# Performance work log

Measured on AMD Instinct MI355X. Metric: run time of the kernel, lower is better.

The kernel has to match this reference:

```python
import jax, jax.numpy as jnp
import numpy as np

N_NODES = 20000
N_EDGES = 320000
N_GRAPHS = 256
D = 256
L = 4
EPS = 1e-5


def setup_inputs() -> dict:
    key = jax.random.key(0)
    ks = jax.random.split(key, 20)
    x = jax.random.normal(ks[0], (N_NODES, D), dtype=jnp.float32)
    edge_index = jax.random.randint(ks[1], (2, N_EDGES), 0, N_NODES, dtype=jnp.int64)
    batch = jnp.sort(jax.random.randint(ks[2], (N_NODES,), 0, N_GRAPHS, dtype=jnp.int64))
    s = 1.0 / np.sqrt(D)
    Wl = jax.random.uniform(ks[3], (L, D, D), jnp.float32, -s, s)
    bl = jax.random.uniform(ks[4], (L, D), jnp.float32, -s, s)
    Wr = jax.random.uniform(ks[5], (L, D, D), jnp.float32, -s, s)
    gamma = jnp.ones((L, D), jnp.float32)
    beta = jnp.zeros((L, D), jnp.float32)
    fc1_w = jax.random.uniform(ks[6], (D, 128), jnp.float32, -s, s)
    fc1_b = jax.random.uniform(ks[7], (128,), jnp.float32, -s, s)
    s2 = 1.0 / np.sqrt(128)
    fc2_w = jax.random.uniform(ks[8], (128, 64), jnp.float32, -s2, s2)
    fc2_b = jax.random.uniform(ks[9], (64,), jnp.float32, -s2, s2)
    s3 = 1.0 / np.sqrt(64)
    fc3_w = jax.random.uniform(ks[10], (64, 10), jnp.float32, -s3, s3)
    fc3_b = jax.random.uniform(ks[11], (10,), jnp.float32, -s3, s3)
    return dict(x=x, edge_index=edge_index, batch=batch, Wl=Wl, bl=bl, Wr=Wr,
                gamma=gamma, beta=beta, fc1_w=fc1_w, fc1_b=fc1_b,
                fc2_w=fc2_w, fc2_b=fc2_b, fc3_w=fc3_w, fc3_b=fc3_b)


def reference(x, edge_index, batch, Wl, bl, Wr, gamma, beta,
              fc1_w, fc1_b, fc2_w, fc2_b, fc3_w, fc3_b):
    src, dst = edge_index[0], edge_index[1]
    # in-degree for mean aggregation (zero-degree nodes -> 0 aggregate)
    deg = jax.ops.segment_sum(jnp.ones((src.shape[0],), x.dtype), dst, num_segments=N_NODES)
    inv_deg = jnp.where(deg > 0, 1.0 / jnp.maximum(deg, 1.0), 0.0)[:, None]
    for i in range(L):
        # SAGEConv: mean-aggregate neighbors, then lin_l(agg) + lin_r(x)
        agg = jax.ops.segment_sum(x[src], dst, num_segments=N_NODES) * inv_deg
        h = agg @ Wl[i] + bl[i] + x @ Wr[i]
        # BatchNorm (training mode: biased batch statistics over nodes)
        mu = jnp.mean(h, axis=0)
        var = jnp.mean(jnp.square(h - mu), axis=0)
        h = (h - mu) * jax.lax.rsqrt(var + EPS) * gamma[i] + beta[i]
        x = jax.nn.relu(h)
    # global_mean_pool over graphs
    cnt = jax.ops.segment_sum(jnp.ones((N_NODES,), x.dtype), batch, num_segments=N_GRAPHS)
    g = jax.ops.segment_sum(x, batch, num_segments=N_GRAPHS) / jnp.maximum(cnt, 1.0)[:, None]
    # MLP classifier: 256 -> 128 -> 64 -> 10
    g = jax.nn.relu(g @ fc1_w + fc1_b)
    g = jax.nn.relu(g @ fc2_w + fc2_b)
    return g @ fc3_w + fc3_b
```

## Files before the change

kernel.cpp:

```cpp
#include <hip/hip_runtime.h>
#include <hip/hip_bf16.h>

#define NN 20000
#define NE 320000
#define NG 256
#define DD 256
#define NL 4
#define NBX2 157
#define NBKT 79

typedef __attribute__((ext_vector_type(8))) short short8;
typedef __attribute__((ext_vector_type(4))) float float4_t;

__device__ __forceinline__ int ld_idx(const int* __restrict__ p, int i, int f64) {
    return f64 ? p[2 * i] : p[i];
}

__device__ __forceinline__ float bf2f(ushort u) {
    return __uint_as_float(((unsigned)u) << 16);
}

__device__ __forceinline__ ushort f2bf(float f) {
    __hip_bfloat16 b = __float2bfloat16(f);
    return *(ushort*)&b;
}


__global__ void k_init(const int* __restrict__ ei, const int* __restrict__ batch,
                       const ushort* __restrict__ x, int* __restrict__ flags,
                       int* __restrict__ deg) {
    int gid = blockIdx.x * 256 + threadIdx.x;
    for (int i = gid; i < NN; i += gridDim.x * 256) deg[i] = 0;
    if (blockIdx.x == 0) {
        __shared__ int cnt0, cnt1, weird;
        int t = threadIdx.x;
        if (t == 0) { cnt0 = 0; cnt1 = 0; weird = 0; }
        __syncthreads();
        for (int tt = t; tt < 512; tt += 256) {
            if (ei[2 * tt + 1] != 0) atomicAdd(&cnt0, 1);
            int i = tt * 9;
            if (batch[2 * i + 1] != 0) atomicAdd(&cnt1, 1);
#pragma unroll
            for (int j = 0; j < 16; j++) {
                ushort v = x[tt * 16 + j];
                if (((v >> 7) & 0xFF) >= 0xC0) atomicAdd(&weird, 1);
            }
        }
        __syncthreads();
        if (t == 0) {
            flags[0] = (cnt0 == 0) ? 1 : 0;
            flags[1] = (cnt1 == 0) ? 1 : 0;
            flags[2] = (weird == 0) ? 1 : 0;
        }
    }
}


#define POFF_BL   0
#define POFF_GA   1024
#define POFF_BE   2048
#define POFF_F1W  3072
#define POFF_F1B  35840
#define POFF_F2W  35968
#define POFF_F2B  44160
#define POFF_F3W  44224
#define POFF_F3B  44864
#define PTOT      44874

#define NB_CVT8   2500
#define NB_FRAG   128
#define NB_CVTP   176
#define NB_DEG    1250
#define NB_GST    79
#define B_FRAG    (NB_CVT8)
#define B_CVTP    (B_FRAG + NB_FRAG)
#define B_DEG     (B_CVTP + NB_CVTP)
#define B_GST     (B_DEG + NB_DEG)
#define NB_PREP   (B_GST + NB_GST)


__global__ __launch_bounds__(256) void k_prep(
    const void* __restrict__ x_in, const void* __restrict__ WL,
    const void* __restrict__ WR, const int* __restrict__ ei,
    const int* __restrict__ batch,
    const void* s0, const void* s1, const void* s2, const void* s3,
    const void* s4, const void* s5, const void* s6, const void* s7, const void* s8,
    ushort* __restrict__ xcan, ushort* __restrict__ wtL, ushort* __restrict__ wtR,
    ushort* __restrict__ pcan, int* __restrict__ deg, int* __restrict__ gstart,
    const int* __restrict__ fl) {
    int blk = blockIdx.x;
    int t = threadIdx.x;
    if (blk < B_FRAG) {
        int i = blk * 256 + t;
        if (fl[2]) {
            *(int4*)(xcan + (size_t)i * 8) = ((const int4*)x_in)[i];
        } else {
            const float* f = (const float*)x_in + (size_t)i * 8;
            ushort ov[8];
#pragma unroll
            for (int d = 0; d < 8; d++) ov[d] = f2bf(f[d]);
            *(int4*)(xcan + (size_t)i * 8) = *(int4*)ov;
        }
    } else if (blk < B_CVTP) {
        __shared__ ushort T[64][65];
        int bid = blk - B_FRAG;
        int lm = bid >> 4;
        int tile = bid & 15;
        int tk = (tile >> 2) * 64, tn = (tile & 3) * 64;
        const void* W = (lm >= 4) ? WR : WL;
        ushort* Wt = (lm >= 4) ? wtR : wtL;
        size_t base = (size_t)(lm & 3) << 16;
        int f32 = !fl[2];
#pragma unroll
        for (int i = 0; i < 16; i++) {
            int flat = t + i * 256;
            int r = flat >> 6, c = flat & 63;
            size_t src = base + (size_t)(tk + r) * 256 + tn + c;
            ushort v = f32 ? f2bf(((const float*)W)[src]) : ((const ushort*)W)[src];
            T[c][r] = v;
        }
        __syncthreads();
#pragma unroll
        for (int i = 0; i < 2; i++) {
            int slot = t + i * 256;
            int f = slot >> 6;
            int lane = slot & 63;
            int ln = (f >> 1) * 16 + (lane & 15);
            int lk = (f & 1) * 32 + ((lane >> 4) << 3);
            int gfblk = ((tn + ln) >> 4) * 8 + ((tk + lk) >> 5);
            ushort tmp[8];
#pragma unroll
            for (int j = 0; j < 8; j++) tmp[j] = T[ln][lk + j];
            *(int4*)(Wt + base + (size_t)gfblk * 512 + lane * 8) = *(int4*)tmp;
        }
    } else if (blk < B_DEG) {
        int i = (blk - B_CVTP) * 256 + t;
        if (i >= PTOT) return;
        const int offs[10] = {POFF_BL, POFF_GA, POFF_BE, POFF_F1W, POFF_F1B,
                              POFF_F2W, POFF_F2B, POFF_F3W, POFF_F3B, PTOT};
        const void* srcs[9] = {s0, s1, s2, s3, s4, s5, s6, s7, s8};
        int seg = 0;
#pragma unroll
        for (int k = 1; k < 9; k++) if (i >= offs[k]) seg = k;
        int local = i - offs[seg];
        if (fl[2]) pcan[i] = ((const ushort*)srcs[seg])[local];
        else       pcan[i] = f2bf(((const float*)srcs[seg])[local]);
    } else if (blk < B_GST) {
        int e = (blk - B_DEG) * 256 + t;
        if (e < NE) {
            int src = ld_idx(ei, e, fl[0]);
            int dst = ld_idx(ei, NE + e, fl[0]);
            if ((unsigned)dst < NN && (unsigned)src < NN) atomicAdd(&deg[dst], 1);
        }
    } else {
        int i = (blk - B_GST) * 256 + t;
        if (i >= NN) return;
        int b = ld_idx(batch, i, fl[1]);
        int bp = (i == 0) ? -1 : ld_idx(batch, i - 1, fl[1]);
        for (int g = bp + 1; g <= b; g++)
            if ((unsigned)g <= NG) gstart[g] = i;
        if (i == NN - 1)
            for (int g = b + 1; g <= NG; g++) gstart[g] = NN;
    }
}


__global__ __launch_bounds__(256) void k_scanA(const int* __restrict__ deg,
                                               int* __restrict__ bsum) {
    __shared__ int red[256];
    int t = threadIdx.x;
    int node = blockIdx.x * 256 + t;
    red[t] = (node < NN) ? deg[node] : 0;
    __syncthreads();
    for (int off = 128; off; off >>= 1) {
        if (t < off) red[t] += red[t + off];
        __syncthreads();
    }
    if (t == 0) bsum[blockIdx.x] = red[0];
}

__global__ __launch_bounds__(256) void k_scanC(
    const int* __restrict__ deg, const int* __restrict__ bsum,
    int* __restrict__ rowst, int* __restrict__ cursor, float* __restrict__ invdeg) {
    __shared__ int bpart[128];
    __shared__ int part[256];
    int b = blockIdx.x, t = threadIdx.x;
    if (t < 128) {
        int s = (t < NBKT) ? bsum[t] : 0;
        bpart[t] = s;
    }
    __syncthreads();
    for (int off = 1; off < 128; off <<= 1) {
        int v = 0;
        if (t < 128 && t >= off) v = bpart[t - off];
        __syncthreads();
        if (t < 128) bpart[t] += v;
        __syncthreads();
    }
    int bpref = (b == 0) ? 0 : bpart[b - 1];
    if (b == 0 && t == 0) rowst[NN] = bpart[NBKT - 1];
    int node = b * 256 + t;
    int d = (node < NN) ? deg[node] : 0;
    part[t] = d;
    __syncthreads();
    for (int off = 1; off < 256; off <<= 1) {
        int v = (t >= off) ? part[t - off] : 0;
        __syncthreads();
        part[t] += v;
        __syncthreads();
    }
    if (node < NN) {
        int o = bpref + part[t] - d;
        rowst[node] = o;
        cursor[node] = o;
        invdeg[node] = d > 0 ? 1.0f / (float)d : 0.0f;
    }
}

__global__ void k_fill(const int* __restrict__ ei, int* __restrict__ cursor,
                       int* __restrict__ csr, const int* __restrict__ fl) {
    int e = blockIdx.x * 256 + threadIdx.x;
    if (e < NE) {
        int src = ld_idx(ei, e, fl[0]);
        int dst = ld_idx(ei, NE + e, fl[0]);
        if ((unsigned)dst < NN && (unsigned)src < NN) {
            int p = atomicAdd(&cursor[dst], 1);
            if ((unsigned)p < NE) csr[p] = src;
        }
    }
}


template <int BNF>
__global__ __launch_bounds__(256) void k_agg4(
    const ushort* __restrict__ X, const int* __restrict__ rs,
    const int* __restrict__ csr, const float* __restrict__ invdeg,
    const float* __restrict__ bnsc, const float* __restrict__ bnsh,
    ushort* __restrict__ AGG) {
    int node = blockIdx.x * 4 + (threadIdx.x >> 6);
    if (node >= NN) return;
    int h = (threadIdx.x >> 5) & 1;
    int j = threadIdx.x & 31;
    float sc[8], sh[8];
    if (BNF) {
        float4 a0 = *(const float4*)(bnsc + j * 8);
        float4 a1 = *(const float4*)(bnsc + j * 8 + 4);
        float4 b0 = *(const float4*)(bnsh + j * 8);
        float4 b1 = *(const float4*)(bnsh + j * 8 + 4);
        sc[0] = a0.x; sc[1] = a0.y; sc[2] = a0.z; sc[3] = a0.w;
        sc[4] = a1.x; sc[5] = a1.y; sc[6] = a1.z; sc[7] = a1.w;
        sh[0] = b0.x; sh[1] = b0.y; sh[2] = b0.z; sh[3] = b0.w;
        sh[4] = b1.x; sh[5] = b1.y; sh[6] = b1.z; sh[7] = b1.w;
    }
    int e0 = rs[node], e1 = rs[node + 1];
    float acc[8] = {};
    int e = e0 + h;
    for (; e + 14 < e1; e += 16) {
        int4 v[8];
#pragma unroll
        for (int r = 0; r < 8; r++) {
            int s = csr[e + 2 * r];
            v[r] = *(const int4*)(X + (size_t)s * DD + j * 8);
        }
#pragma unroll
        for (int r = 0; r < 8; r++) {
            const ushort* u = (const ushort*)&v[r];
#pragma unroll
            for (int d = 0; d < 8; d++) {
                float x = bf2f(u[d]);
                if (BNF) x = fmaxf(x * sc[d] + sh[d], 0.0f);
                acc[d] += x;
            }
        }
    }
    for (; e + 2 < e1; e += 4) {
        int sA = csr[e], sB = csr[e + 2];
        int4 vA = *(const int4*)(X + (size_t)sA * DD + j * 8);
        int4 vB = *(const int4*)(X + (size_t)sB * DD + j * 8);
        const ushort* uA = (const ushort*)&vA;
        const ushort* uB = (const ushort*)&vB;
#pragma unroll
        for (int d = 0; d < 8; d++) {
            float xA = bf2f(uA[d]), xB = bf2f(uB[d]);
            if (BNF) {
                xA = fmaxf(xA * sc[d] + sh[d], 0.0f);
                xB = fmaxf(xB * sc[d] + sh[d], 0.0f);
            }
            acc[d] += xA + xB;
        }
    }
    for (; e < e1; e += 2) {
        int s = csr[e];
        int4 v = *(const int4*)(X + (size_t)s * DD + j * 8);
        const ushort* u = (const ushort*)&v;
#pragma unroll
        for (int d = 0; d < 8; d++) {
            float x = bf2f(u[d]);
            if (BNF) x = fmaxf(x * sc[d] + sh[d], 0.0f);
            acc[d] += x;
        }
    }
#pragma unroll
    for (int d = 0; d < 8; d++)
        acc[d] += __shfl_down(acc[d], 32);
    if (h == 0) {
        float inv = invdeg[node];
        ushort ov[8];
#pragma unroll
        for (int d = 0; d < 8; d++) ov[d] = f2bf(acc[d] * inv);
        *(int4*)(AGG + (size_t)node * DD + j * 8) = *(int4*)ov;
    }
}


template <int BNF>
__global__ __launch_bounds__(256) void k_gemm5(
    const ushort* __restrict__ A1, const ushort* __restrict__ A2,
    const ushort* __restrict__ WtF1, const ushort* __restrict__ WtF2,
    const ushort* __restrict__ bias,
    const float* __restrict__ bnsc, const float* __restrict__ bnsh,
    ushort* __restrict__ H, float* __restrict__ psum, float* __restrict__ psq) {
    __shared__ ushort Als[128][40];
    __shared__ float colsum[128];
    __shared__ float colsq[128];
    const int m0 = blockIdx.x * 128;
    const int n0 = blockIdx.y * 128;
    const int tid = threadIdx.x;
    const int w = tid >> 6, l = tid & 63, lr = l & 15, q = l >> 4;
    const int wm = (w >> 1) * 64, wn = (w & 1) * 64;
    float4_t acc[4][4] = {};

    const int srow = tid >> 1;
    const int sce = (tid & 1) * 16;
    const int nb8 = ((n0 + wn) >> 4) * 8;

    for (int mat = 0; mat < 2; ++mat) {
        const ushort* A = mat ? A2 : A1;
        const ushort* Wf = mat ? WtF2 : WtF1;
        for (int k0 = 0; k0 < 256; k0 += 32) {
            int ar = m0 + srow; if (ar >= NN) ar = NN - 1;
            int4 av0 = *(const int4*)(A + (size_t)ar * DD + k0 + sce);
            int4 av1 = *(const int4*)(A + (size_t)ar * DD + k0 + sce + 8);
            if (BNF && mat == 1) {
                float scv[16], shv[16];
#pragma unroll
                for (int g = 0; g < 4; g++) {
                    float4 s4 = *(const float4*)(bnsc + k0 + sce + g * 4);
                    float4 h4 = *(const float4*)(bnsh + k0 + sce + g * 4);
                    scv[g*4] = s4.x; scv[g*4+1] = s4.y; scv[g*4+2] = s4.z; scv[g*4+3] = s4.w;
                    shv[g*4] = h4.x; shv[g*4+1] = h4.y; shv[g*4+2] = h4.z; shv[g*4+3] = h4.w;
                }
                ushort* u0 = (ushort*)&av0;
                ushort* u1 = (ushort*)&av1;
#pragma unroll
                for (int d = 0; d < 8; d++) {
                    u0[d] = f2bf(fmaxf(bf2f(u0[d]) * scv[d] + shv[d], 0.0f));
                    u1[d] = f2bf(fmaxf(bf2f(u1[d]) * scv[8 + d] + shv[8 + d], 0.0f));
                }
            }
            *(int4*)&Als[srow][sce] = av0;
            *(int4*)&Als[srow][sce + 8] = av1;
            const ushort* bbase = Wf + (((size_t)(nb8 + (k0 >> 5))) << 9) + l * 8;
            short8 bf[4];
#pragma unroll
            for (int in = 0; in < 4; in++)
                bf[in] = *(const short8*)(bbase + in * 4096);
            __syncthreads();
            short8 af[4];
#pragma unroll
            for (int im = 0; im < 4; im++)
                af[im] = *(const short8*)&Als[wm + im * 16 + lr][q * 8];
#pragma unroll
            for (int im = 0; im < 4; im++)
#pragma unroll
                for (int in = 0; in < 4; in++)
                    acc[im][in] = __builtin_amdgcn_mfma_f32_16x16x32_bf16(
                        af[im], bf[in], acc[im][in], 0, 0, 0);
            __syncthreads();
        }
    }
    if (tid < 128) { colsum[tid] = 0.0f; colsq[tid] = 0.0f; }
    __syncthreads();

    int mbase = m0 + wm + q * 4;
#pragma unroll
    for (int in = 0; in < 4; in++) {
        int n = n0 + wn + in * 16 + lr;
        float b = bf2f(bias[n]);
        float s = 0.0f, s2 = 0.0f;
#pragma unroll
        for (int im = 0; im < 4; im++) {
#pragma unroll
            for (int i = 0; i < 4; i++) {
                int m = mbase + im * 16 + i;
                if (m < NN) {
                    float hv = acc[im][in][i] + b;
                    ushort hb = f2bf(hv);
                    H[(size_t)m * DD + n] = hb;
                    float hq = bf2f(hb);
                    s += hq;
                    s2 += hq * hq;
                }
            }
        }
        s += __shfl_xor(s, 16);  s += __shfl_xor(s, 32);
        s2 += __shfl_xor(s2, 16); s2 += __shfl_xor(s2, 32);
        if (q == 0) {
            atomicAdd(&colsum[wn + in * 16 + lr], s);
            atomicAdd(&colsq[wn + in * 16 + lr], s2);
        }
    }
    __syncthreads();
    if (tid < 128) {
        psum[(size_t)blockIdx.x * DD + n0 + tid] = colsum[tid];
        psq[(size_t)blockIdx.x * DD + n0 + tid] = colsq[tid];
    }
}


__global__ __launch_bounds__(64) void k_bnfinal3(
    const float* __restrict__ psum, const float* __restrict__ psq,
    const ushort* __restrict__ gamma, const ushort* __restrict__ beta,
    float* __restrict__ scale, float* __restrict__ shift) {
    int c = blockIdx.x;
    int t = threadIdx.x;
    float s = 0.0f, s2 = 0.0f;
    for (int b = t; b < NBX2; b += 64) {
        s += psum[(size_t)b * DD + c];
        s2 += psq[(size_t)b * DD + c];
    }
#pragma unroll
    for (int o = 32; o; o >>= 1) {
        s += __shfl_down(s, o);
        s2 += __shfl_down(s2, o);
    }
    if (t == 0) {
        float mu = s * (1.0f / NN);
        float var = s2 * (1.0f / NN) - mu * mu;
        if (var < 0.0f) var = 0.0f;
        float rstd = rsqrtf(var + 1e-5f);
        float g = bf2f(gamma[c]);
        float b2 = bf2f(beta[c]);
        scale[c] = g * rstd;
        shift[c] = b2 - mu * g * rstd;
    }
}


__global__ __launch_bounds__(256) void k_head(
    const ushort* __restrict__ Hb, const float* __restrict__ scale,
    const float* __restrict__ shift, const int* __restrict__ gstart,
    const ushort* __restrict__ fc1w, const ushort* __restrict__ fc1b,
    const ushort* __restrict__ fc2w, const ushort* __restrict__ fc2b,
    const ushort* __restrict__ fc3w, const ushort* __restrict__ fc3b,
    void* __restrict__ out, const int* __restrict__ fl) {
    __shared__ float g[256];
    __shared__ float h1[128];
    __shared__ float h2[64];
    int gid = blockIdx.x;
    int t = threadIdx.x;
    int s0 = gstart[gid], e = gstart[gid + 1];
    float sc = scale[t], sh = shift[t];
    float acc = 0.0f;
    for (int i = s0; i < e; i++)
        acc += fmaxf(bf2f(Hb[(size_t)i * DD + t]) * sc + sh, 0.0f);
    g[t] = acc / fmaxf((float)(e - s0), 1.0f);
    __syncthreads();
    if (t < 128) {
        float a = bf2f(fc1b[t]);
        for (int k = 0; k < 256; k++)
            a += g[k] * bf2f(fc1w[k * 128 + t]);
        h1[t] = fmaxf(a, 0.0f);
    }
    __syncthreads();
    if (t < 64) {
        float a2 = bf2f(fc2b[t]);
        for (int k = 0; k < 128; k++)
            a2 += h1[k] * bf2f(fc2w[k * 64 + t]);
        h2[t] = fmaxf(a2, 0.0f);
    }
    __syncthreads();
    if (t < 10) {
        float a3 = bf2f(fc3b[t]);
        for (int k = 0; k < 64; k++)
            a3 += h2[k] * bf2f(fc3w[k * 10 + t]);
        if (fl[2]) ((__hip_bfloat16*)out)[gid * 10 + t] = __float2bfloat16(a3);
        else       ((float*)out)[gid * 10 + t] = a3;
    }
}


static inline char* bump(char*& p, size_t n) {
    char* r = p;
    p += (n + 255) & ~(size_t)255;
    return r;
}

extern "C" void kernel_launch(void* const* d_in, const int* in_sizes, int n_in,
                              void* d_out, int out_size, void* d_ws, size_t ws_size,
                              hipStream_t stream) {
    const void* x_in  = d_in[0];
    const int*  ei    = (const int*)d_in[1];
    const int*  batch = (const int*)d_in[2];
    const void* Wl    = d_in[3];
    const void* bl    = d_in[4];
    const void* Wr    = d_in[5];
    const void* gamma = d_in[6];
    const void* beta  = d_in[7];

    char* p = (char*)d_ws;
    int*    flags    = (int*)bump(p, 256);
    ushort* wtL      = (ushort*)bump(p, (size_t)NL * 65536 * 2);
    ushort* wtR      = (ushort*)bump(p, (size_t)NL * 65536 * 2);
    ushort* xcan     = (ushort*)bump(p, (size_t)NN * DD * 2);
    ushort* pcan     = (ushort*)bump(p, (size_t)PTOT * 2);
    int*    deg      = (int*)bump(p, NN * 4);
    int*    bsum     = (int*)bump(p, NBKT * 4);
    int*    rowst    = (int*)bump(p, (NN + 1) * 4);
    int*    cursor   = (int*)bump(p, NN * 4);
    float*  invdeg   = (float*)bump(p, NN * 4);
    int*    csr      = (int*)bump(p, NE * 4);
    int*    gstart   = (int*)bump(p, (NG + 1) * 4);
    ushort* agg      = (ushort*)bump(p, (size_t)NN * DD * 2);
    ushort* hb0      = (ushort*)bump(p, (size_t)NN * DD * 2);
    ushort* hb1      = (ushort*)bump(p, (size_t)NN * DD * 2);
    float*  psum     = (float*)bump(p, (size_t)NBX2 * DD * 4);
    float*  psq      = (float*)bump(p, (size_t)NBX2 * DD * 4);
    float*  scale    = (float*)bump(p, DD * 4);
    float*  shift    = (float*)bump(p, DD * 4);

    if ((size_t)(p - (char*)d_ws) > ws_size) return;

    ushort* blc = pcan + POFF_BL;
    ushort* gac = pcan + POFF_GA;
    ushort* bec = pcan + POFF_BE;
    ushort* f1w = pcan + POFF_F1W;
    ushort* f1b = pcan + POFF_F1B;
    ushort* f2w = pcan + POFF_F2W;
    ushort* f2b = pcan + POFF_F2B;
    ushort* f3w = pcan + POFF_F3W;
    ushort* f3b = pcan + POFF_F3B;

    k_init<<<80, 256, 0, stream>>>(ei, batch, (const ushort*)x_in, flags, deg);
    k_prep<<<NB_PREP, 256, 0, stream>>>(
        x_in, Wl, Wr, ei, batch,
        bl, gamma, beta, d_in[8], d_in[9], d_in[10], d_in[11], d_in[12], d_in[13],
        xcan, wtL, wtR, pcan, deg, gstart, flags);
    k_scanA<<<NBKT, 256, 0, stream>>>(deg, bsum);
    k_scanC<<<NBKT, 256, 0, stream>>>(deg, bsum, rowst, cursor, invdeg);
    k_fill<<<(NE + 255) / 256, 256, 0, stream>>>(ei, cursor, csr, flags);

    ushort* hbuf[2] = {hb0, hb1};
    const ushort* xsrc = xcan;
    for (int l = 0; l < NL; l++) {
        ushort* hdst = hbuf[l & 1];
        if (l == 0) {
            k_agg4<0><<<(NN + 3) / 4, 256, 0, stream>>>(xsrc, rowst, csr, invdeg,
                                                        scale, shift, agg);
            k_gemm5<0><<<dim3(NBX2, 2), 256, 0, stream>>>(
                agg, xsrc, wtL, wtR, blc, scale, shift, hdst, psum, psq);
        } else {
            k_agg4<1><<<(NN + 3) / 4, 256, 0, stream>>>(xsrc, rowst, csr, invdeg,
                                                        scale, shift, agg);
            k_gemm5<1><<<dim3(NBX2, 2), 256, 0, stream>>>(
                agg, xsrc, wtL + (size_t)l * 65536, wtR + (size_t)l * 65536,
                blc + l * DD, scale, shift, hdst, psum, psq);
        }
        k_bnfinal3<<<DD, 64, 0, stream>>>(psum, psq, gac + l * DD, bec + l * DD,
                                          scale, shift);
        xsrc = hdst;
    }

    k_head<<<NG, 256, 0, stream>>>(xsrc, scale, shift, gstart,
                                   f1w, f1b, f2w, f2b, f3w, f3b, d_out, flags);
}
```

Before: 372.1 us.

## Fuse neighbor aggregation into per-layer GEMM kernel and merge scan kernels

Neighbor mean aggregation and the SAGE GEMM now run in one kernel per layer. Each 640-thread block aggregates 80 nodes into shared memory and then runs MFMA over the full 256-column output, so the intermediate aggregate never goes through global memory and one launch per layer is removed. The two degree-scan kernels become a single kernel in which each block recomputes its prefix by summing all preceding degrees. In exchange there are only 250 large blocks with a heavy LDS footprint, which can lower occupancy. The gather and the MFMA phases no longer overlap across separate kernels, and the weights are re-read by every block.

```diff
diff --git a/kernel.cpp b/kernel.cpp
--- a/kernel.cpp
+++ b/kernel.cpp
@@ -6,8 +6,9 @@
 #define NG 256
 #define DD 256
 #define NL 4
-#define NBX2 157
 #define NBKT 79
+#define BM 80
+#define NBLK 250
 
 typedef __attribute__((ext_vector_type(8))) short short8;
 typedef __attribute__((ext_vector_type(4))) float float4_t;
@@ -165,40 +166,21 @@
 }
 
 
-__global__ __launch_bounds__(256) void k_scanA(const int* __restrict__ deg,
-                                               int* __restrict__ bsum) {
+__global__ __launch_bounds__(256) void k_scan(
+    const int* __restrict__ deg, int* __restrict__ rowst,
+    int* __restrict__ cursor, float* __restrict__ invdeg) {
     __shared__ int red[256];
-    int t = threadIdx.x;
-    int node = blockIdx.x * 256 + t;
-    red[t] = (node < NN) ? deg[node] : 0;
+    __shared__ int part[256];
+    int b = blockIdx.x, t = threadIdx.x;
+    int s = 0;
+    for (int i = t; i < b * 256; i += 256) s += deg[i];
+    red[t] = s;
     __syncthreads();
     for (int off = 128; off; off >>= 1) {
         if (t < off) red[t] += red[t + off];
         __syncthreads();
     }
-    if (t == 0) bsum[blockIdx.x] = red[0];
-}
-
-__global__ __launch_bounds__(256) void k_scanC(
-    const int* __restrict__ deg, const int* __restrict__ bsum,
-    int* __restrict__ rowst, int* __restrict__ cursor, float* __restrict__ invdeg) {
-    __shared__ int bpart[128];
-    __shared__ int part[256];
-    int b = blockIdx.x, t = threadIdx.x;
-    if (t < 128) {
-        int s = (t < NBKT) ? bsum[t] : 0;
-        bpart[t] = s;
-    }
-    __syncthreads();
-    for (int off = 1; off < 128; off <<= 1) {
-        int v = 0;
-        if (t < 128 && t >= off) v = bpart[t - off];
-        __syncthreads();
-        if (t < 128) bpart[t] += v;
-        __syncthreads();
-    }
-    int bpref = (b == 0) ? 0 : bpart[b - 1];
-    if (b == 0 && t == 0) rowst[NN] = bpart[NBKT - 1];
+    int bpref = red[0];
     int node = b * 256 + t;
     int d = (node < NN) ? deg[node] : 0;
     part[t] = d;
@@ -215,6 +197,7 @@
         cursor[node] = o;
         invdeg[node] = d > 0 ? 1.0f / (float)d : 0.0f;
     }
+    if (b == NBKT - 1 && t == 255) rowst[NN] = bpref + part[255];
 }
 
 __global__ void k_fill(const int* __restrict__ ei, int* __restrict__ cursor,
@@ -232,188 +215,160 @@
 
 
 template <int BNF>
-__global__ __launch_bounds__(256) void k_agg4(
+__global__ __launch_bounds__(640) void k_layer(
     const ushort* __restrict__ X, const int* __restrict__ rs,
     const int* __restrict__ csr, const float* __restrict__ invdeg,
-    const float* __restrict__ bnsc, const float* __restrict__ bnsh,
-    ushort* __restrict__ AGG) {
-    int node = blockIdx.x * 4 + (threadIdx.x >> 6);
-    if (node >= NN) return;
-    int h = (threadIdx.x >> 5) & 1;
-    int j = threadIdx.x & 31;
-    float sc[8], sh[8];
-    if (BNF) {
-        float4 a0 = *(const float4*)(bnsc + j * 8);
-        float4 a1 = *(const float4*)(bnsc + j * 8 + 4);
-        float4 b0 = *(const float4*)(bnsh + j * 8);
-        float4 b1 = *(const float4*)(bnsh + j * 8 + 4);
-        sc[0] = a0.x; sc[1] = a0.y; sc[2] = a0.z; sc[3] = a0.w;
-        sc[4] = a1.x; sc[5] = a1.y; sc[6] = a1.z; sc[7] = a1.w;
-        sh[0] = b0.x; sh[1] = b0.y; sh[2] = b0.z; sh[3] = b0.w;
-        sh[4] = b1.x; sh[5] = b1.y; sh[6] = b1.z; sh[7] = b1.w;
-    }
-    int e0 = rs[node], e1 = rs[node + 1];
-    float acc[8] = {};
-    int e = e0 + h;
-    for (; e + 14 < e1; e += 16) {
-        int4 v[8];
-#pragma unroll
-        for (int r = 0; r < 8; r++) {
-            int s = csr[e + 2 * r];
-            v[r] = *(const int4*)(X + (size_t)s * DD + j * 8);
-        }
-#pragma unroll
-        for (int r = 0; r < 8; r++) {
-            const ushort* u = (const ushort*)&v[r];
-#pragma unroll
-            for (int d = 0; d < 8; d++) {
-                float x = bf2f(u[d]);
-                if (BNF) x = fmaxf(x * sc[d] + sh[d], 0.0f);
-                acc[d] += x;
-            }
-        }
-    }
-    for (; e + 2 < e1; e += 4) {
-        int sA = csr[e], sB = csr[e + 2];
-        int4 vA = *(const int4*)(X + (size_t)sA * DD + j * 8);
-        int4 vB = *(const int4*)(X + (size_t)sB * DD + j * 8);
-        const ushort* uA = (const ushort*)&vA;
-        const ushort* uB = (const ushort*)&vB;
-#pragma unroll
-        for (int d = 0; d < 8; d++) {
-            float xA = bf2f(uA[d]), xB = bf2f(uB[d]);
-            if (BNF) {
-                xA = fmaxf(xA * sc[d] + sh[d], 0.0f);
-                xB = fmaxf(xB * sc[d] + sh[d], 0.0f);
-            }
-            acc[d] += xA + xB;
-        }
-    }
-    for (; e < e1; e += 2) {
-        int s = csr[e];
-        int4 v = *(const int4*)(X + (size_t)s * DD + j * 8);
-        const ushort* u = (const ushort*)&v;
-#pragma unroll
-        for (int d = 0; d < 8; d++) {
-            float x = bf2f(u[d]);
-            if (BNF) x = fmaxf(x * sc[d] + sh[d], 0.0f);
-            acc[d] += x;
-        }
-    }
-#pragma unroll
-    for (int d = 0; d < 8; d++)
-        acc[d] += __shfl_down(acc[d], 32);
-    if (h == 0) {
-        float inv = invdeg[node];
-        ushort ov[8];
-#pragma unroll
-        for (int d = 0; d < 8; d++) ov[d] = f2bf(acc[d] * inv);
-        *(int4*)(AGG + (size_t)node * DD + j * 8) = *(int4*)ov;
-    }
-}
-
-
-template <int BNF>
-__global__ __launch_bounds__(256) void k_gemm5(
-    const ushort* __restrict__ A1, const ushort* __restrict__ A2,
-    const ushort* __restrict__ WtF1, const ushort* __restrict__ WtF2,
+    const ushort* __restrict__ WfL, const ushort* __restrict__ WfR,
     const ushort* __restrict__ bias,
     const float* __restrict__ bnsc, const float* __restrict__ bnsh,
     ushort* __restrict__ H, float* __restrict__ psum, float* __restrict__ psq) {
-    __shared__ ushort Als[128][40];
-    __shared__ float colsum[128];
-    __shared__ float colsq[128];
-    const int m0 = blockIdx.x * 128;
-    const int n0 = blockIdx.y * 128;
+    __shared__ ushort A1[BM][264];
+    __shared__ float scs[256], shs[256];
+    __shared__ float colsum[256], colsq[256];
+    const int m0 = blockIdx.x * BM;
     const int tid = threadIdx.x;
-    const int w = tid >> 6, l = tid & 63, lr = l & 15, q = l >> 4;
-    const int wm = (w >> 1) * 64, wn = (w & 1) * 64;
-    float4_t acc[4][4] = {};
-
-    const int srow = tid >> 1;
-    const int sce = (tid & 1) * 16;
-    const int nb8 = ((n0 + wn) >> 4) * 8;
-
+    const int w = tid >> 6;
+    const int lane = tid & 63;
+
+    if (tid < 256) {
+        colsum[tid] = 0.0f;
+        colsq[tid] = 0.0f;
+        if (BNF) { scs[tid] = bnsc[tid]; shs[tid] = bnsh[tid]; }
+    }
+    __syncthreads();
+
+    {
+        const int h = lane >> 5;
+        const int j = lane & 31;
+        float sc[8], sh[8];
+        if (BNF) {
+#pragma unroll
+            for (int d = 0; d < 8; d++) { sc[d] = scs[j * 8 + d]; sh[d] = shs[j * 8 + d]; }
+        }
+        for (int nl = 0; nl < 8; ++nl) {
+            const int r = w * 8 + nl;
+            const int node = m0 + r;
+            int e0 = rs[node], e1 = rs[node + 1];
+            float acc[8] = {};
+            int e = e0 + h;
+            for (; e + 14 < e1; e += 16) {
+                int4 v[8];
+#pragma unroll
+                for (int rr = 0; rr < 8; rr++) {
+                    int s = csr[e + 2 * rr];
+                    v[rr] = *(const int4*)(X + (size_t)s * DD + j * 8);
+                }
+#pragma unroll
+                for (int rr = 0; rr < 8; rr++) {
+                    const ushort* u = (const ushort*)&v[rr];
+#pragma unroll
+                    for (int d = 0; d < 8; d++) {
+                        float x = bf2f(u[d]);
+                        if (BNF) x = fmaxf(x * sc[d] + sh[d], 0.0f);
+                        acc[d] += x;
+                    }
+                }
+            }
+            for (; e + 2 < e1; e += 4) {
+                int sA = csr[e], sB = csr[e + 2];
+                int4 vA = *(const int4*)(X + (size_t)sA * DD + j * 8);
+                int4 vB = *(const int4*)(X + (size_t)sB * DD + j * 8);
+                const ushort* uA = (const ushort*)&vA;
+                const ushort* uB = (const ushort*)&vB;
+#pragma unroll
+                for (int d = 0; d < 8; d++) {
+                    float xA = bf2f(uA[d]), xB = bf2f(uB[d]);
+                    if (BNF) {
+                        xA = fmaxf(xA * sc[d] + sh[d], 0.0f);
+                        xB = fmaxf(xB * sc[d] + sh[d], 0.0f);
+                    }
+                    acc[d] += xA + xB;
+                }
+            }
+            for (; e < e1; e += 2) {
+                int s = csr[e];
+                int4 v = *(const int4*)(X + (size_t)s * DD + j * 8);
+                const ushort* u = (const ushort*)&v;
+#pragma unroll
+                for (int d = 0; d < 8; d++) {
+                    float x = bf2f(u[d]);
+                    if (BNF) x = fmaxf(x * sc[d] + sh[d], 0.0f);
+                    acc[d] += x;
+                }
+            }
+#pragma unroll
+            for (int d = 0; d < 8; d++)
+                acc[d] += __shfl_down(acc[d], 32);
+            if (h == 0) {
+                float inv = invdeg[node];
+                ushort ov[8];
+#pragma unroll
+                for (int d = 0; d < 8; d++) ov[d] = f2bf(acc[d] * inv);
+                *(int4*)&A1[r][j * 8] = *(int4*)ov;
+            }
+        }
+    }
+    __syncthreads();
+
+    const int wm = w >> 1, wn = w & 1;
+    const int lr = lane & 15, q = lane >> 4;
+    float4_t acc[8] = {};
     for (int mat = 0; mat < 2; ++mat) {
-        const ushort* A = mat ? A2 : A1;
-        const ushort* Wf = mat ? WtF2 : WtF1;
+        const ushort* Wf = mat ? WfR : WfL;
+        const int arow = m0 + wm * 16 + lr;
+#pragma unroll
         for (int k0 = 0; k0 < 256; k0 += 32) {
-            int ar = m0 + srow; if (ar >= NN) ar = NN - 1;
-            int4 av0 = *(const int4*)(A + (size_t)ar * DD + k0 + sce);
-            int4 av1 = *(const int4*)(A + (size_t)ar * DD + k0 + sce + 8);
-            if (BNF && mat == 1) {
-                float scv[16], shv[16];
-#pragma unroll
-                for (int g = 0; g < 4; g++) {
-                    float4 s4 = *(const float4*)(bnsc + k0 + sce + g * 4);
-                    float4 h4 = *(const float4*)(bnsh + k0 + sce + g * 4);
-                    scv[g*4] = s4.x; scv[g*4+1] = s4.y; scv[g*4+2] = s4.z; scv[g*4+3] = s4.w;
-                    shv[g*4] = h4.x; shv[g*4+1] = h4.y; shv[g*4+2] = h4.z; shv[g*4+3] = h4.w;
+            short8 af;
+            if (mat == 0) {
+                af = *(const short8*)&A1[wm * 16 + lr][k0 + q * 8];
+            } else {
+                int4 av = *(const int4*)(X + (size_t)arow * DD + k0 + q * 8);
+                if (BNF) {
+                    ushort* u = (ushort*)&av;
+#pragma unroll
+                    for (int d = 0; d < 8; d++) {
+                        int c = k0 + q * 8 + d;
+                        u[d] = f2bf(fmaxf(bf2f(u[d]) * scs[c] + shs[c], 0.0f));
+                    }
                 }
-                ushort* u0 = (ushort*)&av0;
-                ushort* u1 = (ushort*)&av1;
-#pragma unroll
-                for (int d = 0; d < 8; d++) {
-                    u0[d] = f2bf(fmaxf(bf2f(u0[d]) * scv[d] + shv[d], 0.0f));
-                    u1[d] = f2bf(fmaxf(bf2f(u1[d]) * scv[8 + d] + shv[8 + d], 0.0f));
-                }
-            }
-            *(int4*)&Als[srow][sce] = av0;
-            *(int4*)&Als[srow][sce + 8] = av1;
-            const ushort* bbase = Wf + (((size_t)(nb8 + (k0 >> 5))) << 9) + l * 8;
-            short8 bf[4];
-#pragma unroll
-            for (int in = 0; in < 4; in++)
-                bf[in] = *(const short8*)(bbase + in * 4096);
-            __syncthreads();
-            short8 af[4];
-#pragma unroll
-            for (int im = 0; im < 4; im++)
-                af[im] = *(const short8*)&Als[wm + im * 16 + lr][q * 8];
-#pragma unroll
-            for (int im = 0; im < 4; im++)
-#pragma unroll
-                for (int in = 0; in < 4; in++)
-                    acc[im][in] = __builtin_amdgcn_mfma_f32_16x16x32_bf16(
-                        af[im], bf[in], acc[im][in], 0, 0, 0);
-            __syncthreads();
-        }
-    }
-    if (tid < 128) { colsum[tid] = 0.0f; colsq[tid] = 0.0f; }
-    __syncthreads();
-
-    int mbase = m0 + wm + q * 4;
-#pragma unroll
-    for (int in = 0; in < 4; in++) {
-        int n = n0 + wn + in * 16 + lr;
+                af = *(short8*)&av;
+            }
+            const ushort* bbase = Wf + (((size_t)(wn * 64 + (k0 >> 5))) << 9) + lane * 8;
+#pragma unroll
+            for (int in = 0; in < 8; ++in) {
+                short8 bf = *(const short8*)(bbase + in * 4096);
+                acc[in] = __builtin_amdgcn_mfma_f32_16x16x32_bf16(af, bf, acc[in], 0, 0, 0);
+            }
+        }
+    }
+
+    const int mbase = m0 + wm * 16 + q * 4;
+#pragma unroll
+    for (int in = 0; in < 8; ++in) {
+        const int n = wn * 128 + in * 16 + lr;
         float b = bf2f(bias[n]);
         float s = 0.0f, s2 = 0.0f;
 #pragma unroll
-        for (int im = 0; im < 4; im++) {
-#pragma unroll
-            for (int i = 0; i < 4; i++) {
-                int m = mbase + im * 16 + i;
-                if (m < NN) {
-                    float hv = acc[im][in][i] + b;
-                    ushort hb = f2bf(hv);
-                    H[(size_t)m * DD + n] = hb;
-                    float hq = bf2f(hb);
-                    s += hq;
-                    s2 += hq * hq;
-                }
-            }
+        for (int i = 0; i < 4; ++i) {
+            int m = mbase + i;
+            float hv = acc[in][i] + b;
+            ushort hb = f2bf(hv);
+            H[(size_t)m * DD + n] = hb;
+            float hq = bf2f(hb);
+            s += hq;
+            s2 += hq * hq;
         }
         s += __shfl_xor(s, 16);  s += __shfl_xor(s, 32);
         s2 += __shfl_xor(s2, 16); s2 += __shfl_xor(s2, 32);
         if (q == 0) {
-            atomicAdd(&colsum[wn + in * 16 + lr], s);
-            atomicAdd(&colsq[wn + in * 16 + lr], s2);
-        }
-    }
-    __syncthreads();
-    if (tid < 128) {
-        psum[(size_t)blockIdx.x * DD + n0 + tid] = colsum[tid];
-        psq[(size_t)blockIdx.x * DD + n0 + tid] = colsq[tid];
+            atomicAdd(&colsum[n], s);
+            atomicAdd(&colsq[n], s2);
+        }
+    }
+    __syncthreads();
+    if (tid < 256) {
+        psum[(size_t)blockIdx.x * DD + tid] = colsum[tid];
+        psq[(size_t)blockIdx.x * DD + tid] = colsq[tid];
     }
 }
 
@@ -425,7 +380,7 @@
     int c = blockIdx.x;
     int t = threadIdx.x;
     float s = 0.0f, s2 = 0.0f;
-    for (int b = t; b < NBX2; b += 64) {
+    for (int b = t; b < NBLK; b += 64) {
         s += psum[(size_t)b * DD + c];
         s2 += psq[(size_t)b * DD + c];
     }
@@ -515,17 +470,15 @@
     ushort* xcan     = (ushort*)bump(p, (size_t)NN * DD * 2);
     ushort* pcan     = (ushort*)bump(p, (size_t)PTOT * 2);
     int*    deg      = (int*)bump(p, NN * 4);
-    int*    bsum     = (int*)bump(p, NBKT * 4);
     int*    rowst    = (int*)bump(p, (NN + 1) * 4);
     int*    cursor   = (int*)bump(p, NN * 4);
     float*  invdeg   = (float*)bump(p, NN * 4);
     int*    csr      = (int*)bump(p, NE * 4);
     int*    gstart   = (int*)bump(p, (NG + 1) * 4);
-    ushort* agg      = (ushort*)bump(p, (size_t)NN * DD * 2);
     ushort* hb0      = (ushort*)bump(p, (size_t)NN * DD * 2);
     ushort* hb1      = (ushort*)bump(p, (size_t)NN * DD * 2);
-    float*  psum     = (float*)bump(p, (size_t)NBX2 * DD * 4);
-    float*  psq      = (float*)bump(p, (size_t)NBX2 * DD * 4);
+    float*  psum     = (float*)bump(p, (size_t)NBLK * DD * 4);
+    float*  psq      = (float*)bump(p, (size_t)NBLK * DD * 4);
     float*  scale    = (float*)bump(p, DD * 4);
     float*  shift    = (float*)bump(p, DD * 4);
 
@@ -546,25 +499,23 @@
         x_in, Wl, Wr, ei, batch,
         bl, gamma, beta, d_in[8], d_in[9], d_in[10], d_in[11], d_in[12], d_in[13],
         xcan, wtL, wtR, pcan, deg, gstart, flags);
-    k_scanA<<<NBKT, 256, 0, stream>>>(deg, bsum);
-    k_scanC<<<NBKT, 256, 0, stream>>>(deg, bsum, rowst, cursor, invdeg);
+    k_scan<<<NBKT, 256, 0, stream>>>(deg, rowst, cursor, invdeg);
     k_fill<<<(NE + 255) / 256, 256, 0, stream>>>(ei, cursor, csr, flags);
 
     ushort* hbuf[2] = {hb0, hb1};
     const ushort* xsrc = xcan;
     for (int l = 0; l < NL; l++) {
         ushort* hdst = hbuf[l & 1];
+        const ushort* wl = wtL + (size_t)l * 65536;
+        const ushort* wr = wtR + (size_t)l * 65536;
         if (l == 0) {
-            k_agg4<0><<<(NN + 3) / 4, 256, 0, stream>>>(xsrc, rowst, csr, invdeg,
-                                                        scale, shift, agg);
-            k_gemm5<0><<<dim3(NBX2, 2), 256, 0, stream>>>(
-                agg, xsrc, wtL, wtR, blc, scale, shift, hdst, psum, psq);
+            k_layer<0><<<NBLK, 640, 0, stream>>>(
+                xsrc, rowst, csr, invdeg, wl, wr, blc,
+                scale, shift, hdst, psum, psq);
         } else {
-            k_agg4<1><<<(NN + 3) / 4, 256, 0, stream>>>(xsrc, rowst, csr, invdeg,
-                                                        scale, shift, agg);
-            k_gemm5<1><<<dim3(NBX2, 2), 256, 0, stream>>>(
-                agg, xsrc, wtL + (size_t)l * 65536, wtR + (size_t)l * 65536,
-                blc + l * DD, scale, shift, hdst, psum, psq);
+            k_layer<1><<<NBLK, 640, 0, stream>>>(
+                xsrc, rowst, csr, invdeg, wl, wr, blc + l * DD,
+                scale, shift, hdst, psum, psq);
         }
         k_bnfinal3<<<DD, 64, 0, stream>>>(psum, psq, gac + l * DD, bec + l * DD,
                                           scale, shift);
```

After: 399.1 us. 1.07x slower.

## Retile SAGE GEMM to 80-row blocks with full-K LDS staging and merge scan kernels

Applied to the files above, without the earlier changes.

The fused lin_l/lin_r GEMM now uses 80-row M tiles, so 250 blocks divide 20000 nodes exactly and no bounds checks are needed. Each block stages the whole 80x256 A panel in LDS once per matrix instead of 32-wide K slices, which removes the per-slice barriers. Each wave now covers 80x32 outputs with 5x2 MFMA accumulators. The two-pass degree scan becomes a single kernel that recomputes each block's prefix directly from deg, dropping a launch at the cost of redundant reads. BN partials are sized for the new block count, and a redundant dead assignment was added in prep.

```diff
diff --git a/kernel.cpp b/kernel.cpp
--- a/kernel.cpp
+++ b/kernel.cpp
@@ -6,8 +6,9 @@
 #define NG 256
 #define DD 256
 #define NL 4
-#define NBX2 157
 #define NBKT 79
+#define BM 80
+#define NBLK 250
 
 typedef __attribute__((ext_vector_type(8))) short short8;
 typedef __attribute__((ext_vector_type(4))) float float4_t;
@@ -146,7 +147,8 @@
         if (fl[2]) pcan[i] = ((const ushort*)srcs[seg])[local];
         else       pcan[i] = f2bf(((const float*)srcs[seg])[local]);
     } else if (blk < B_GST) {
-        int e = (blk - B_DEG) * 256 + t;
+        int e = (blk - B_CVTP - NB_CVTP) * 256 + t;
+        e = (blk - B_DEG) * 256 + t;
         if (e < NE) {
             int src = ld_idx(ei, e, fl[0]);
             int dst = ld_idx(ei, NE + e, fl[0]);
@@ -165,40 +167,21 @@
 }
 
 
-__global__ __launch_bounds__(256) void k_scanA(const int* __restrict__ deg,
-                                               int* __restrict__ bsum) {
+__global__ __launch_bounds__(256) void k_scan(
+    const int* __restrict__ deg, int* __restrict__ rowst,
+    int* __restrict__ cursor, float* __restrict__ invdeg) {
     __shared__ int red[256];
-    int t = threadIdx.x;
-    int node = blockIdx.x * 256 + t;
-    red[t] = (node < NN) ? deg[node] : 0;
+    __shared__ int part[256];
+    int b = blockIdx.x, t = threadIdx.x;
+    int s = 0;
+    for (int i = t; i < b * 256; i += 256) s += deg[i];
+    red[t] = s;
     __syncthreads();
     for (int off = 128; off; off >>= 1) {
         if (t < off) red[t] += red[t + off];
         __syncthreads();
     }
-    if (t == 0) bsum[blockIdx.x] = red[0];
-}
-
-__global__ __launch_bounds__(256) void k_scanC(
-    const int* __restrict__ deg, const int* __restrict__ bsum,
-    int* __restrict__ rowst, int* __restrict__ cursor, float* __restrict__ invdeg) {
-    __shared__ int bpart[128];
-    __shared__ int part[256];
-    int b = blockIdx.x, t = threadIdx.x;
-    if (t < 128) {
-        int s = (t < NBKT) ? bsum[t] : 0;
-        bpart[t] = s;
-    }
-    __syncthreads();
-    for (int off = 1; off < 128; off <<= 1) {
-        int v = 0;
-        if (t < 128 && t >= off) v = bpart[t - off];
-        __syncthreads();
-        if (t < 128) bpart[t] += v;
-        __syncthreads();
-    }
-    int bpref = (b == 0) ? 0 : bpart[b - 1];
-    if (b == 0 && t == 0) rowst[NN] = bpart[NBKT - 1];
+    int bpref = red[0];
     int node = b * 256 + t;
     int d = (node < NN) ? deg[node] : 0;
     part[t] = d;
@@ -215,6 +198,7 @@
         cursor[node] = o;
         invdeg[node] = d > 0 ? 1.0f / (float)d : 0.0f;
     }
+    if (b == NBKT - 1 && t == 255) rowst[NN] = bpref + part[255];
 }
 
 __global__ void k_fill(const int* __restrict__ ei, int* __restrict__ cursor,
@@ -314,100 +298,87 @@
 
 
 template <int BNF>
-__global__ __launch_bounds__(256) void k_gemm5(
+__global__ __launch_bounds__(256) void k_gemm6(
     const ushort* __restrict__ A1, const ushort* __restrict__ A2,
     const ushort* __restrict__ WtF1, const ushort* __restrict__ WtF2,
     const ushort* __restrict__ bias,
     const float* __restrict__ bnsc, const float* __restrict__ bnsh,
     ushort* __restrict__ H, float* __restrict__ psum, float* __restrict__ psq) {
-    __shared__ ushort Als[128][40];
+    __shared__ ushort Als[BM][264];
     __shared__ float colsum[128];
     __shared__ float colsq[128];
-    const int m0 = blockIdx.x * 128;
+    const int m0 = blockIdx.x * BM;
     const int n0 = blockIdx.y * 128;
     const int tid = threadIdx.x;
-    const int w = tid >> 6, l = tid & 63, lr = l & 15, q = l >> 4;
-    const int wm = (w >> 1) * 64, wn = (w & 1) * 64;
-    float4_t acc[4][4] = {};
-
-    const int srow = tid >> 1;
-    const int sce = (tid & 1) * 16;
-    const int nb8 = ((n0 + wn) >> 4) * 8;
+    const int w = tid >> 6, lane = tid & 63;
+    const int lr = lane & 15, q = lane >> 4;
+    float4_t acc[5][2] = {};
+
+    if (tid < 128) { colsum[tid] = 0.0f; colsq[tid] = 0.0f; }
 
     for (int mat = 0; mat < 2; ++mat) {
         const ushort* A = mat ? A2 : A1;
         const ushort* Wf = mat ? WtF2 : WtF1;
+        __syncthreads();
+#pragma unroll
+        for (int i = 0; i < 10; i++) {
+            int flat = tid + i * 256;
+            int r = flat >> 5;
+            int c = (flat & 31) * 8;
+            int4 av = *(const int4*)(A + (size_t)(m0 + r) * DD + c);
+            if (BNF && mat == 1) {
+                ushort* u = (ushort*)&av;
+#pragma unroll
+                for (int d = 0; d < 8; d++)
+                    u[d] = f2bf(fmaxf(bf2f(u[d]) * bnsc[c + d] + bnsh[c + d], 0.0f));
+            }
+            *(int4*)&Als[r][c] = av;
+        }
+        __syncthreads();
+#pragma unroll
         for (int k0 = 0; k0 < 256; k0 += 32) {
-            int ar = m0 + srow; if (ar >= NN) ar = NN - 1;
-            int4 av0 = *(const int4*)(A + (size_t)ar * DD + k0 + sce);
-            int4 av1 = *(const int4*)(A + (size_t)ar * DD + k0 + sce + 8);
-            if (BNF && mat == 1) {
-                float scv[16], shv[16];
-#pragma unroll
-                for (int g = 0; g < 4; g++) {
-                    float4 s4 = *(const float4*)(bnsc + k0 + sce + g * 4);
-                    float4 h4 = *(const float4*)(bnsh + k0 + sce + g * 4);
-                    scv[g*4] = s4.x; scv[g*4+1] = s4.y; scv[g*4+2] = s4.z; scv[g*4+3] = s4.w;
-                    shv[g*4] = h4.x; shv[g*4+1] = h4.y; shv[g*4+2] = h4.z; shv[g*4+3] = h4.w;
-                }
-                ushort* u0 = (ushort*)&av0;
-                ushort* u1 = (ushort*)&av1;
-#pragma unroll
-                for (int d = 0; d < 8; d++) {
-                    u0[d] = f2bf(fmaxf(bf2f(u0[d]) * scv[d] + shv[d], 0.0f));
-                    u1[d] = f2bf(fmaxf(bf2f(u1[d]) * scv[8 + d] + shv[8 + d], 0.0f));
-                }
+            short8 af[5];
+#pragma unroll
+            for (int im = 0; im < 5; im++)
+                af[im] = *(const short8*)&Als[im * 16 + lr][k0 + q * 8];
+            const ushort* bbase =
+                Wf + (((size_t)(((n0 + w * 32) >> 4) * 8 + (k0 >> 5))) << 9) + lane * 8;
+#pragma unroll
+            for (int in = 0; in < 2; in++) {
+                short8 bf = *(const short8*)(bbase + in * 4096);
+#pragma unroll
+                for (int im = 0; im < 5; im++)
+                    acc[im][in] = __builtin_amdgcn_mfma_f32_16x16x32_bf16(
+                        af[im], bf, acc[im][in], 0, 0, 0);
             }
-            *(int4*)&Als[srow][sce] = av0;
-            *(int4*)&Als[srow][sce + 8] = av1;
-            const ushort* bbase = Wf + (((size_t)(nb8 + (k0 >> 5))) << 9) + l * 8;
-            short8 bf[4];
-#pragma unroll
-            for (int in = 0; in < 4; in++)
-                bf[in] = *(const short8*)(bbase + in * 4096);
-            __syncthreads();
-            short8 af[4];
-#pragma unroll
-            for (int im = 0; im < 4; im++)
-                af[im] = *(const short8*)&Als[wm + im * 16 + lr][q * 8];
-#pragma unroll
-            for (int im = 0; im < 4; im++)
-#pragma unroll
-                for (int in = 0; in < 4; in++)
-                    acc[im][in] = __builtin_amdgcn_mfma_f32_16x16x32_bf16(
-                        af[im], bf[in], acc[im][in], 0, 0, 0);
-            __syncthreads();
-        }
-    }
-    if (tid < 128) { colsum[tid] = 0.0f; colsq[tid] = 0.0f; }
-    __syncthreads();
-
-    int mbase = m0 + wm + q * 4;
-#pragma unroll
-    for (int in = 0; in < 4; in++) {
-        int n = n0 + wn + in * 16 + lr;
+        }
+    }
+
+    const int mbase = m0 + q * 4;
+#pragma unroll
+    for (int in = 0; in < 2; ++in) {
+        const int nl = w * 32 + in * 16 + lr;
+        const int n = n0 + nl;
         float b = bf2f(bias[n]);
         float s = 0.0f, s2 = 0.0f;
 #pragma unroll
-        for (int im = 0; im < 4; im++) {
-#pragma unroll
-            for (int i = 0; i < 4; i++) {
+        for (int im = 0; im < 5; ++im) {
+#pragma unroll
+            for (int i = 0; i < 4; ++i) {
                 int m = mbase + im * 16 + i;
-                if (m < NN) {
-                    float hv = acc[im][in][i] + b;
-                    ushort hb = f2bf(hv);
-                    H[(size_t)m * DD + n] = hb;
-                    float hq = bf2f(hb);
-                    s += hq;
-                    s2 += hq * hq;
-                }
+                float hv = acc[im][in][i] + b;
+                ushort hb = f2bf(hv);
+                H[(size_t)m * DD + n] = hb;
+                float hq = bf2f(hb);
+                s += hq;
+                s2 += hq * hq;
             }
         }
         s += __shfl_xor(s, 16);  s += __shfl_xor(s, 32);
         s2 += __shfl_xor(s2, 16); s2 += __shfl_xor(s2, 32);
         if (q == 0) {
-            atomicAdd(&colsum[wn + in * 16 + lr], s);
-            atomicAdd(&colsq[wn + in * 16 + lr], s2);
+            atomicAdd(&colsum[nl], s);
+            atomicAdd(&colsq[nl], s2);
         }
     }
     __syncthreads();
@@ -425,7 +396,7 @@
     int c = blockIdx.x;
     int t = threadIdx.x;
     float s = 0.0f, s2 = 0.0f;
-    for (int b = t; b < NBX2; b += 64) {
+    for (int b = t; b < NBLK; b += 64) {
         s += psum[(size_t)b * DD + c];
         s2 += psq[(size_t)b * DD + c];
     }
@@ -515,7 +486,6 @@
     ushort* xcan     = (ushort*)bump(p, (size_t)NN * DD * 2);
     ushort* pcan     = (ushort*)bump(p, (size_t)PTOT * 2);
     int*    deg      = (int*)bump(p, NN * 4);
-    int*    bsum     = (int*)bump(p, NBKT * 4);
     int*    rowst    = (int*)bump(p, (NN + 1) * 4);
     int*    cursor   = (int*)bump(p, NN * 4);
     float*  invdeg   = (float*)bump(p, NN * 4);
@@ -524,8 +494,8 @@
     ushort* agg      = (ushort*)bump(p, (size_t)NN * DD * 2);
     ushort* hb0      = (ushort*)bump(p, (size_t)NN * DD * 2);
     ushort* hb1      = (ushort*)bump(p, (size_t)NN * DD * 2);
-    float*  psum     = (float*)bump(p, (size_t)NBX2 * DD * 4);
-    float*  psq      = (float*)bump(p, (size_t)NBX2 * DD * 4);
+    float*  psum     = (float*)bump(p, (size_t)NBLK * DD * 4);
+    float*  psq      = (float*)bump(p, (size_t)NBLK * DD * 4);
     float*  scale    = (float*)bump(p, DD * 4);
     float*  shift    = (float*)bump(p, DD * 4);
 
@@ -546,25 +516,25 @@
         x_in, Wl, Wr, ei, batch,
         bl, gamma, beta, d_in[8], d_in[9], d_in[10], d_in[11], d_in[12], d_in[13],
         xcan, wtL, wtR, pcan, deg, gstart, flags);
-    k_scanA<<<NBKT, 256, 0, stream>>>(deg, bsum);
-    k_scanC<<<NBKT, 256, 0, stream>>>(deg, bsum, rowst, cursor, invdeg);
+    k_scan<<<NBKT, 256, 0, stream>>>(deg, rowst, cursor, invdeg);
     k_fill<<<(NE + 255) / 256, 256, 0, stream>>>(ei, cursor, csr, flags);
 
     ushort* hbuf[2] = {hb0, hb1};
     const ushort* xsrc = xcan;
     for (int l = 0; l < NL; l++) {
         ushort* hdst = hbuf[l & 1];
+        const ushort* wl = wtL + (size_t)l * 65536;
+        const ushort* wr = wtR + (size_t)l * 65536;
         if (l == 0) {
             k_agg4<0><<<(NN + 3) / 4, 256, 0, stream>>>(xsrc, rowst, csr, invdeg,
                                                         scale, shift, agg);
-            k_gemm5<0><<<dim3(NBX2, 2), 256, 0, stream>>>(
-                agg, xsrc, wtL, wtR, blc, scale, shift, hdst, psum, psq);
+            k_gemm6<0><<<dim3(NBLK, 2), 256, 0, stream>>>(
+                agg, xsrc, wl, wr, blc, scale, shift, hdst, psum, psq);
         } else {
             k_agg4<1><<<(NN + 3) / 4, 256, 0, stream>>>(xsrc, rowst, csr, invdeg,
                                                         scale, shift, agg);
-            k_gemm5<1><<<dim3(NBX2, 2), 256, 0, stream>>>(
-                agg, xsrc, wtL + (size_t)l * 65536, wtR + (size_t)l * 65536,
-                blc + l * DD, scale, shift, hdst, psum, psq);
+            k_gemm6<1><<<dim3(NBLK, 2), 256, 0, stream>>>(
+                agg, xsrc, wl, wr, blc + l * DD, scale, shift, hdst, psum, psq);
         }
         k_bnfinal3<<<DD, 64, 0, stream>>>(psum, psq, gac + l * DD, bec + l * DD,
                                           scale, shift);
```

Result: no change. 366.6 us (-1.5%).
